# Kernel optimization log

Measured on AMD Instinct MI355X. Metric: run time of the kernel, lower is better.

## Reference

```python
import jax, jax.numpy as jnp
import numpy as np

NUM_HEADS = 16
HIDDEN = 1024
ATTN_DIM = 64            # per-head q/k dim
HEAD_OUT = 64            # per-head v dim
OUT_DIM = 1024
BATCH, SEQ = 2, 2048


def setup_inputs() -> dict:
    key = jax.random.key(0)
    ks = jax.random.split(key, 9)
    s_in = 1.0 / np.sqrt(HIDDEN)
    s_o = 1.0 / np.sqrt(NUM_HEADS * HEAD_OUT)
    return {
        "x": jax.random.normal(ks[0], (BATCH, SEQ, HIDDEN), dtype=jnp.float32),
        # Linear weights stored [in, out] so y = x @ W + b
        "Wq": jax.random.uniform(ks[1], (HIDDEN, NUM_HEADS * ATTN_DIM), jnp.float32, -s_in, s_in),
        "bq": jax.random.uniform(ks[2], (NUM_HEADS * ATTN_DIM,), jnp.float32, -s_in, s_in),
        "Wk": jax.random.uniform(ks[3], (HIDDEN, NUM_HEADS * ATTN_DIM), jnp.float32, -s_in, s_in),
        "bk": jax.random.uniform(ks[4], (NUM_HEADS * ATTN_DIM,), jnp.float32, -s_in, s_in),
        "Wv": jax.random.uniform(ks[5], (HIDDEN, NUM_HEADS * HEAD_OUT), jnp.float32, -s_in, s_in),
        "bv": jax.random.uniform(ks[6], (HIDDEN, NUM_HEADS * HEAD_OUT)[1:], jnp.float32, -s_in, s_in),
        "Wo": jax.random.uniform(ks[7], (NUM_HEADS * HEAD_OUT, OUT_DIM), jnp.float32, -s_o, s_o),
        "bo": jax.random.uniform(ks[8], (OUT_DIM,), jnp.float32, -s_o, s_o),
    }


def _split_heads(y, h):
    b, s, _ = y.shape
    return y.reshape(b, s, h, -1).transpose(0, 2, 1, 3)  # [b, h, s, d]


def reference(x, Wq, bq, Wk, bk, Wv, bv, Wo, bo):
    h = NUM_HEADS
    q = _split_heads(x @ Wq + bq, h)                    # [b,h,s,dq]
    k = _split_heads(x @ Wk + bk, h)                    # [b,h,s,dq]
    v = _split_heads(x @ Wv + bv, h)                    # [b,h,s,dv]
    scale = 1.0 / jnp.sqrt(jnp.float32(ATTN_DIM))
    # pattern[b,h,i,j] = key_i . query_j  (i=key index, j=query index)
    pattern = jnp.einsum('bhid,bhjd->bhij', k, q) * scale
    # softmax over key axis (dim=-2), matching t.softmax(..., dim=-2)
    prob = jax.nn.softmax(pattern, axis=-2)             # [b,h,key,query]
    # out[b,h,s,d] = sum_i prob[b,h,i,s] * v[b,h,i,d]
    out = jnp.einsum('bhis,bhid->bhsd', prob, v)        # [b,h,s,dv]
    b, _, s, dv = out.shape
    concat = out.transpose(0, 2, 1, 3).reshape(b, s, h * dv)
    return concat @ Wo + bo
```

## Files before the change

kernel.cpp:

```cpp
#include <hip/hip_runtime.h>
#include <cstdint>
#include <cstddef>

using f16   = _Float16;
using f16x4 = __attribute__((ext_vector_type(4))) _Float16;
using f16x8 = __attribute__((ext_vector_type(8))) _Float16;
using f32x4 = __attribute__((ext_vector_type(4))) float;

__device__ __forceinline__ f32x4 mfma16(f16x8 a, f16x8 b, f32x4 c) {
  return __builtin_amdgcn_mfma_f32_16x16x32_f16(a, b, c, 0, 0, 0);
}

__device__ __forceinline__ void gld16(const f16* g, f16* l) {
  __builtin_amdgcn_global_load_lds(
      (__attribute__((address_space(1))) void*)g,
      (__attribute__((address_space(3))) void*)l, 16, 0, 0);
}

constexpr int BATCH = 2, SEQL = 2048, HID = 1024, NH = 16, DH = 64;
constexpr int TOK = BATCH * SEQL;
constexpr int NQKV = 3 * HID;

__global__ __launch_bounds__(256) void k_convert_x(const float* __restrict__ x,
                                                   f16* __restrict__ xh) {
  int i = (blockIdx.x * 256 + threadIdx.x) * 4;
  float4 v = *(const float4*)(x + i);
  f16x4 o = { (f16)v.x, (f16)v.y, (f16)v.z, (f16)v.w };
  *(f16x4*)(xh + i) = o;
}

__global__ __launch_bounds__(256) void k_transpose(const float* __restrict__ Wq,
                                                   const float* __restrict__ Wk,
                                                   const float* __restrict__ Wv,
                                                   const float* __restrict__ Wo,
                                                   f16* __restrict__ WT,
                                                   f16* __restrict__ WoT) {
  __shared__ float tile[32][33];
  int mat = blockIdx.z;
  const float* W = (mat == 0) ? Wq : (mat == 1) ? Wk : (mat == 2) ? Wv : Wo;
  int in0 = blockIdx.x * 32, out0 = blockIdx.y * 32;
  int c = threadIdx.x & 31, r8 = threadIdx.x >> 5;
#pragma unroll
  for (int i = 0; i < 4; i++) {
    int r = r8 + i * 8;
    tile[r][c] = W[(size_t)(in0 + r) * HID + out0 + c];
  }
  __syncthreads();
#pragma unroll
  for (int i = 0; i < 4; i++) {
    int r = r8 + i * 8;
    f16 v = (f16)tile[c][r];
    if (mat == 3) WoT[(size_t)(out0 + r) * HID + in0 + c] = v;
    else          WT[(size_t)(mat * HID + out0 + r) * HID + in0 + c] = v;
  }
}

__global__ __launch_bounds__(256, 2) void k_gemm_qkv(
    const f16* __restrict__ xh, const f16* __restrict__ WT,
    const float* __restrict__ bq, const float* __restrict__ bk,
    const float* __restrict__ bv,
    f16* __restrict__ Qh, f16* __restrict__ Kh, f16* __restrict__ Vp) {
  constexpr int K = HID;
  int m0 = blockIdx.x * 128, n0 = blockIdx.y * 128;
  int tid = threadIdx.x;
  int w = tid >> 6, lane = tid & 63, lr = lane & 15, lq = lane >> 4;
  int wm = w >> 1, wn = w & 1;
  __shared__ f16 Ash[128 * 32];
  __shared__ f16 Bsh[128 * 32];
  f32x4 acc[4][4];
#pragma unroll
  for (int i = 0; i < 4; i++)
#pragma unroll
    for (int j = 0; j < 4; j++) acc[i][j] = (f32x4){0.f, 0.f, 0.f, 0.f};

  int row0 = tid >> 2, seg0 = tid & 3;
  int row1 = (256 + tid) >> 2;
  const f16* Ag0 = xh + (size_t)(m0 + row0) * K + seg0 * 8;
  const f16* Ag1 = xh + (size_t)(m0 + row1) * K + seg0 * 8;
  const f16* Bg0 = WT + (size_t)(n0 + row0) * K + seg0 * 8;
  const f16* Bg1 = WT + (size_t)(n0 + row1) * K + seg0 * 8;

  for (int k0 = 0; k0 < K; k0 += 32) {
    __syncthreads();
    gld16(Ag0 + k0, Ash + tid * 8);
    gld16(Ag1 + k0, Ash + (256 + tid) * 8);
    gld16(Bg0 + k0, Bsh + tid * 8);
    gld16(Bg1 + k0, Bsh + (256 + tid) * 8);
    __syncthreads();
    f16x8 af[4], bfr[4];
#pragma unroll
    for (int mt = 0; mt < 4; mt++)
      af[mt] = *(const f16x8*)(Ash + (wm * 64 + mt * 16 + lr) * 32 + lq * 8);
#pragma unroll
    for (int nt = 0; nt < 4; nt++)
      bfr[nt] = *(const f16x8*)(Bsh + (wn * 64 + nt * 16 + lr) * 32 + lq * 8);
#pragma unroll
    for (int mt = 0; mt < 4; mt++)
#pragma unroll
      for (int nt = 0; nt < 4; nt++)
        acc[mt][nt] = mfma16(af[mt], bfr[nt], acc[mt][nt]);
  }

#pragma unroll
  for (int nt = 0; nt < 4; nt++) {
    int o = n0 + wn * 64 + nt * 16 + lr;
    int sec = o >> 10, o1 = o & 1023, hh = o1 >> 6, dd = o1 & 63;
    float bias = (sec == 0) ? bq[o1] : (sec == 1) ? bk[o1] : bv[o1];
#pragma unroll
    for (int mt = 0; mt < 4; mt++) {
      int t0 = m0 + wm * 64 + mt * 16 + lq * 4;
      int b = t0 >> 11, s0 = t0 & (SEQL - 1);
      size_t bh = (size_t)(b * NH + hh);
      if (sec == 2) {
        f16x4 pv = { (f16)(acc[mt][nt][0] + bias), (f16)(acc[mt][nt][1] + bias),
                     (f16)(acc[mt][nt][2] + bias), (f16)(acc[mt][nt][3] + bias) };
        int pb = (s0 & ~31) | ((s0 & 12) << 1) | ((s0 >> 2) & 4);
        *(f16x4*)(Vp + (bh * DH + dd) * SEQL + pb) = pv;
      } else {
        f16* dst = (sec == 0) ? Qh : Kh;
#pragma unroll
        for (int r = 0; r < 4; r++)
          dst[(bh * SEQL + s0 + r) * DH + dd] = (f16)(acc[mt][nt][r] + bias);
      }
    }
  }
}

__global__ __launch_bounds__(256, 2) void k_attn(const f16* __restrict__ Qh,
                                                 const f16* __restrict__ Kh,
                                                 const f16* __restrict__ Vp,
                                                 f16* __restrict__ Ao) {
  int bh = blockIdx.x;
  int qblk = blockIdx.y;
  int b = bh >> 4, h = bh & 15;
  int tid = threadIdx.x;
  int w = tid >> 6;
  int g = w >> 1;
  int wq = w & 1;
  int lane = tid & 63, lr = lane & 15, lq = lane >> 4;

  __shared__ f16 sh[8 * 64 * 64];

  f16x8 qf[4][2];
#pragma unroll
  for (int qt = 0; qt < 4; qt++) {
    const f16* Qbase =
        Qh + ((size_t)bh * SEQL + qblk * 128 + wq * 64 + qt * 16 + lr) * DH;
#pragma unroll
    for (int ks = 0; ks < 2; ks++) {
      qf[qt][ks] = *(const f16x8*)(Qbase + ks * 32 + lq * 8);
      qf[qt][ks] = qf[qt][ks] * (f16)0.18033688f;
    }
  }

  f32x4 O[4][4];
#pragma unroll
  for (int qt = 0; qt < 4; qt++)
#pragma unroll
    for (int dt = 0; dt < 4; dt++) O[qt][dt] = (f32x4){0.f, 0.f, 0.f, 0.f};
  float lsum[4] = {0.f, 0.f, 0.f, 0.f};

  int sg = w >> 1, skv = w & 1;
  int srow8 = lane >> 3;
  int scol = ((lane & 7) ^ srow8) * 8;
  const f16* sgl;
  size_t pstride, kbstride;
  if (skv == 0) {
    sgl = Kh + ((size_t)bh * SEQL + sg * 1024 + srow8) * DH + scol;
    pstride = (size_t)8 * DH;
    kbstride = (size_t)64 * DH;
  } else {
    sgl = Vp + ((size_t)bh * DH + srow8) * SEQL + sg * 1024 + scol;
    pstride = (size_t)8 * SEQL;
    kbstride = (size_t)64;
  }
  f16* sdst0 = sh + ((sg * 2 + 0) * 2 + skv) * 4096 + lane * 8;
  f16* sdst1 = sh + ((sg * 2 + 1) * 2 + skv) * 4096 + lane * 8;

  int swz = lr & 7;
  int c0 = ((0 * 4 + lq) ^ swz) * 8;
  int c1 = ((1 * 4 + lq) ^ swz) * 8;

  {
    const f16* src = sgl;
#pragma unroll
    for (int p8 = 0; p8 < 8; p8++) gld16(src + p8 * pstride, sdst0 + p8 * 512);
  }

  for (int kb = 0; kb < 16; kb++) {
    __syncthreads();
    if (kb < 15) {
      const f16* src = sgl + (size_t)(kb + 1) * kbstride;
      f16* sdst = ((kb + 1) & 1) ? sdst1 : sdst0;
#pragma unroll
      for (int p8 = 0; p8 < 8; p8++) gld16(src + p8 * pstride, sdst + p8 * 512);
    }

    const f16* Kp = sh + ((g * 2 + (kb & 1)) * 2 + 0) * 4096;
    const f16* Vq = Kp + 4096;

    f32x4 sacc[4][4];
#pragma unroll
    for (int qt = 0; qt < 4; qt++)
#pragma unroll
      for (int kt = 0; kt < 4; kt++) sacc[qt][kt] = (f32x4){0.f, 0.f, 0.f, 0.f};
    __builtin_amdgcn_s_setprio(1);
#pragma unroll
    for (int ks = 0; ks < 2; ks++) {
      int kc = ks ? c1 : c0;
#pragma unroll
      for (int kt = 0; kt < 4; kt++) {
        f16x8 kf = *(const f16x8*)(Kp + (kt * 16 + lr) * 64 + kc);
        sacc[0][kt] = mfma16(kf, qf[0][ks], sacc[0][kt]);
        sacc[1][kt] = mfma16(kf, qf[1][ks], sacc[1][kt]);
        sacc[2][kt] = mfma16(kf, qf[2][ks], sacc[2][kt]);
        sacc[3][kt] = mfma16(kf, qf[3][ks], sacc[3][kt]);
      }
    }
    __builtin_amdgcn_s_setprio(0);

    f16x8 pf[4][2];
#pragma unroll
    for (int qt = 0; qt < 4; qt++) {
      float part = 0.f;
#pragma unroll
      for (int kt = 0; kt < 4; kt++) {
        float p0 = __builtin_amdgcn_exp2f(sacc[qt][kt][0]);
        float p1 = __builtin_amdgcn_exp2f(sacc[qt][kt][1]);
        float p2 = __builtin_amdgcn_exp2f(sacc[qt][kt][2]);
        float p3 = __builtin_amdgcn_exp2f(sacc[qt][kt][3]);
        part += (p0 + p1) + (p2 + p3);
        int s = kt >> 1, off = (kt & 1) * 4;
        pf[qt][s][off + 0] = (f16)p0; pf[qt][s][off + 1] = (f16)p1;
        pf[qt][s][off + 2] = (f16)p2; pf[qt][s][off + 3] = (f16)p3;
      }
      lsum[qt] += part;
    }

    __builtin_amdgcn_s_setprio(1);
#pragma unroll
    for (int s = 0; s < 2; s++) {
      int vc = s ? c1 : c0;
#pragma unroll
      for (int dt = 0; dt < 4; dt++) {
        f16x8 vf = *(const f16x8*)(Vq + (dt * 16 + lr) * 64 + vc);
        O[0][dt] = mfma16(vf, pf[0][s], O[0][dt]);
        O[1][dt] = mfma16(vf, pf[1][s], O[1][dt]);
        O[2][dt] = mfma16(vf, pf[2][s], O[2][dt]);
        O[3][dt] = mfma16(vf, pf[3][s], O[3][dt]);
      }
    }
    __builtin_amdgcn_s_setprio(0);
  }

  __syncthreads();
  float* part = (float*)sh;
  float* plsum = part + 128 * 64;
  if (g == 1) {
#pragma unroll
    for (int qt = 0; qt < 4; qt++) {
      int ql = wq * 64 + qt * 16 + lr;
#pragma unroll
      for (int dt = 0; dt < 4; dt++) {
        int slot = (dt * 4 + lq) ^ lr;
        *(f32x4*)(part + ql * 64 + slot * 4) = O[qt][dt];
      }
      plsum[ql * 4 + lq] = lsum[qt];
    }
  }
  __syncthreads();
  if (g == 0) {
#pragma unroll
    for (int qt = 0; qt < 4; qt++) {
      int ql = wq * 64 + qt * 16 + lr;
      float ls = lsum[qt] + plsum[ql * 4 + lq];
      float l1 = ls + __shfl_xor(ls, 16);
      float ltot = l1 + __shfl_xor(l1, 32);
      float inv = 1.0f / ltot;
      int q = qblk * 128 + ql;
      f16* dst = Ao + ((size_t)b * SEQL + q) * HID + h * DH;
#pragma unroll
      for (int dt = 0; dt < 4; dt++) {
        int slot = (dt * 4 + lq) ^ lr;
        f32x4 po = *(const f32x4*)(part + ql * 64 + slot * 4);
        f16x4 o = { (f16)((O[qt][dt][0] + po[0]) * inv),
                    (f16)((O[qt][dt][1] + po[1]) * inv),
                    (f16)((O[qt][dt][2] + po[2]) * inv),
                    (f16)((O[qt][dt][3] + po[3]) * inv) };
        *(f16x4*)(dst + dt * 16 + lq * 4) = o;
      }
    }
  }
}

__global__ __launch_bounds__(256, 2) void k_gemm_out(const f16* __restrict__ Ah,
                                                     const f16* __restrict__ WoT,
                                                     const float* __restrict__ bo,
                                                     float* __restrict__ out) {
  constexpr int K = HID;
  int m0 = blockIdx.x * 128, n0 = blockIdx.y * 64;
  int tid = threadIdx.x;
  int w = tid >> 6, lane = tid & 63, lr = lane & 15, lq = lane >> 4;
  int wm = w >> 1, wn = w & 1;
  __shared__ f16 Ash[128 * 32];
  __shared__ f16 Bsh[64 * 32];
  f32x4 acc[4][2];
#pragma unroll
  for (int i = 0; i < 4; i++)
#pragma unroll
    for (int j = 0; j < 2; j++) acc[i][j] = (f32x4){0.f, 0.f, 0.f, 0.f};

  int row0 = tid >> 2, seg0 = tid & 3;
  int row1 = (256 + tid) >> 2;
  const f16* Ag0 = Ah + (size_t)(m0 + row0) * K + seg0 * 8;
  const f16* Ag1 = Ah + (size_t)(m0 + row1) * K + seg0 * 8;
  const f16* Bg0 = WoT + (size_t)(n0 + row0) * K + seg0 * 8;

  for (int k0 = 0; k0 < K; k0 += 32) {
    __syncthreads();
    gld16(Ag0 + k0, Ash + tid * 8);
    gld16(Ag1 + k0, Ash + (256 + tid) * 8);
    gld16(Bg0 + k0, Bsh + tid * 8);
    __syncthreads();
    f16x8 af[4], bfr[2];
#pragma unroll
    for (int mt = 0; mt < 4; mt++)
      af[mt] = *(const f16x8*)(Ash + (wm * 64 + mt * 16 + lr) * 32 + lq * 8);
#pragma unroll
    for (int nt = 0; nt < 2; nt++)
      bfr[nt] = *(const f16x8*)(Bsh + (wn * 32 + nt * 16 + lr) * 32 + lq * 8);
#pragma unroll
    for (int mt = 0; mt < 4; mt++)
#pragma unroll
      for (int nt = 0; nt < 2; nt++)
        acc[mt][nt] = mfma16(af[mt], bfr[nt], acc[mt][nt]);
  }

#pragma unroll
  for (int nt = 0; nt < 2; nt++) {
    int o = n0 + wn * 32 + nt * 16 + lr;
    float bias = bo[o];
#pragma unroll
    for (int mt = 0; mt < 4; mt++) {
      int t0 = m0 + wm * 64 + mt * 16 + lq * 4;
#pragma unroll
      for (int r = 0; r < 4; r++)
        out[(size_t)(t0 + r) * HID + o] = acc[mt][nt][r] + bias;
    }
  }
}

extern "C" void kernel_launch(void* const* d_in, const int* in_sizes, int n_in,
                              void* d_out, int out_size, void* d_ws, size_t ws_size,
                              hipStream_t stream) {
  const float* x  = (const float*)d_in[0];
  const float* Wq = (const float*)d_in[1];
  const float* bq = (const float*)d_in[2];
  const float* Wk = (const float*)d_in[3];
  const float* bk = (const float*)d_in[4];
  const float* Wv = (const float*)d_in[5];
  const float* bv = (const float*)d_in[6];
  const float* Wo = (const float*)d_in[7];
  const float* bo = (const float*)d_in[8];

  char* ws = (char*)d_ws;
  f16* xh  = (f16*)(ws + 0);
  f16* WT  = (f16*)(ws + 8388608);
  f16* WoT = (f16*)(ws + 14680064);
  f16* Qh  = (f16*)(ws + 16777216);
  f16* Kh  = (f16*)(ws + 25165824);
  f16* Vp  = (f16*)(ws + 33554432);
  f16* Ao  = (f16*)(ws + 41943040);

  k_convert_x<<<TOK * HID / 1024, 256, 0, stream>>>(x, xh);
  k_transpose<<<dim3(32, 32, 4), 256, 0, stream>>>(Wq, Wk, Wv, Wo, WT, WoT);
  k_gemm_qkv<<<dim3(TOK / 128, NQKV / 128), 256, 0, stream>>>(xh, WT, bq, bk, bv,
                                                              Qh, Kh, Vp);
  k_attn<<<dim3(BATCH * NH, SEQL / 128), 256, 0, stream>>>(Qh, Kh, Vp, Ao);
  k_gemm_out<<<dim3(TOK / 128, HID / 64), 256, 0, stream>>>(Ao, WoT, bo,
                                                            (float*)d_out);
}
```

Before: 180.8 us.

## Fuse all stages into one persistent kernel with software grid barriers

Replaces the five separate launches (convert, transpose, QKV GEMM, attention, output GEMM) with one persistent kernel of 512 blocks that loops over each stage's work items and separates stages with an atomic-counter grid barrier. This aims to remove kernel launch gaps and tail drain between stages. It relies on all 512 blocks being co-resident, and adds barrier spin cost plus a memset for the barrier state.

```diff
diff --git a/kernel.cpp b/kernel.cpp
--- a/kernel.cpp
+++ b/kernel.cpp
@@ -20,332 +20,356 @@
 constexpr int BATCH = 2, SEQL = 2048, HID = 1024, NH = 16, DH = 64;
 constexpr int TOK = BATCH * SEQL;
 constexpr int NQKV = 3 * HID;
-
-__global__ __launch_bounds__(256) void k_convert_x(const float* __restrict__ x,
-                                                   f16* __restrict__ xh) {
-  int i = (blockIdx.x * 256 + threadIdx.x) * 4;
-  float4 v = *(const float4*)(x + i);
-  f16x4 o = { (f16)v.x, (f16)v.y, (f16)v.z, (f16)v.w };
-  *(f16x4*)(xh + i) = o;
-}
-
-__global__ __launch_bounds__(256) void k_transpose(const float* __restrict__ Wq,
-                                                   const float* __restrict__ Wk,
-                                                   const float* __restrict__ Wv,
-                                                   const float* __restrict__ Wo,
-                                                   f16* __restrict__ WT,
-                                                   f16* __restrict__ WoT) {
-  __shared__ float tile[32][33];
-  int mat = blockIdx.z;
-  const float* W = (mat == 0) ? Wq : (mat == 1) ? Wk : (mat == 2) ? Wv : Wo;
-  int in0 = blockIdx.x * 32, out0 = blockIdx.y * 32;
-  int c = threadIdx.x & 31, r8 = threadIdx.x >> 5;
-#pragma unroll
-  for (int i = 0; i < 4; i++) {
-    int r = r8 + i * 8;
-    tile[r][c] = W[(size_t)(in0 + r) * HID + out0 + c];
+constexpr int NBLK = 512;
+
+__device__ __forceinline__ void gbar(unsigned* bar) {
+  __syncthreads();
+  if (threadIdx.x == 0) {
+    __threadfence();
+    unsigned gen = __hip_atomic_load(bar + 1, __ATOMIC_ACQUIRE,
+                                     __HIP_MEMORY_SCOPE_AGENT);
+    unsigned arr = __hip_atomic_fetch_add(bar, 1u, __ATOMIC_ACQ_REL,
+                                          __HIP_MEMORY_SCOPE_AGENT);
+    if (arr == NBLK - 1) {
+      __hip_atomic_store(bar, 0u, __ATOMIC_RELAXED, __HIP_MEMORY_SCOPE_AGENT);
+      __hip_atomic_fetch_add(bar + 1, 1u, __ATOMIC_RELEASE,
+                             __HIP_MEMORY_SCOPE_AGENT);
+    } else {
+      while (__hip_atomic_load(bar + 1, __ATOMIC_ACQUIRE,
+                               __HIP_MEMORY_SCOPE_AGENT) == gen)
+        __builtin_amdgcn_s_sleep(8);
+    }
+    __threadfence();
   }
   __syncthreads();
-#pragma unroll
-  for (int i = 0; i < 4; i++) {
-    int r = r8 + i * 8;
-    f16 v = (f16)tile[c][r];
-    if (mat == 3) WoT[(size_t)(out0 + r) * HID + in0 + c] = v;
-    else          WT[(size_t)(mat * HID + out0 + r) * HID + in0 + c] = v;
+}
+
+__global__ __launch_bounds__(256, 2) void k_fused(
+    const float* __restrict__ x,  const float* __restrict__ Wq,
+    const float* __restrict__ bq, const float* __restrict__ Wk,
+    const float* __restrict__ bk, const float* __restrict__ Wv,
+    const float* __restrict__ bv, const float* __restrict__ Wo,
+    const float* __restrict__ bo, float* __restrict__ out,
+    f16* __restrict__ xh, f16* __restrict__ WT, f16* __restrict__ WoT,
+    f16* __restrict__ Qh, f16* __restrict__ Kh, f16* __restrict__ Vp,
+    f16* __restrict__ Ao, unsigned* __restrict__ bar) {
+  __shared__ __attribute__((aligned(16))) char smem[65536];
+  int bid = blockIdx.x;
+  int tid = threadIdx.x;
+
+  {
+    float (*tile)[33] = (float(*)[33])smem;
+    for (int j = bid; j < 8192; j += NBLK) {
+      if (j < 4096) {
+        int i = j * 1024 + tid * 4;
+        float4 v = *(const float4*)(x + i);
+        f16x4 o = { (f16)v.x, (f16)v.y, (f16)v.z, (f16)v.w };
+        *(f16x4*)(xh + i) = o;
+      } else {
+        int t = j - 4096;
+        int mat = t >> 10, rem = t & 1023;
+        int in0 = (rem >> 5) * 32, out0 = (rem & 31) * 32;
+        const float* W = (mat == 0) ? Wq : (mat == 1) ? Wk
+                        : (mat == 2) ? Wv : Wo;
+        int c = tid & 31, r8 = tid >> 5;
+        __syncthreads();
+#pragma unroll
+        for (int i = 0; i < 4; i++) {
+          int r = r8 + i * 8;
+          tile[r][c] = W[(size_t)(in0 + r) * HID + out0 + c];
+        }
+        __syncthreads();
+#pragma unroll
+        for (int i = 0; i < 4; i++) {
+          int r = r8 + i * 8;
+          f16 v = (f16)tile[c][r];
+          if (mat == 3) WoT[(size_t)(out0 + r) * HID + in0 + c] = v;
+          else          WT[(size_t)(mat * HID + out0 + r) * HID + in0 + c] = v;
+        }
+      }
+    }
   }
-}
-
-__global__ __launch_bounds__(256, 2) void k_gemm_qkv(
-    const f16* __restrict__ xh, const f16* __restrict__ WT,
-    const float* __restrict__ bq, const float* __restrict__ bk,
-    const float* __restrict__ bv,
-    f16* __restrict__ Qh, f16* __restrict__ Kh, f16* __restrict__ Vp) {
-  constexpr int K = HID;
-  int m0 = blockIdx.x * 128, n0 = blockIdx.y * 128;
-  int tid = threadIdx.x;
-  int w = tid >> 6, lane = tid & 63, lr = lane & 15, lq = lane >> 4;
-  int wm = w >> 1, wn = w & 1;
-  __shared__ f16 Ash[128 * 32];
-  __shared__ f16 Bsh[128 * 32];
-  f32x4 acc[4][4];
-#pragma unroll
-  for (int i = 0; i < 4; i++)
-#pragma unroll
-    for (int j = 0; j < 4; j++) acc[i][j] = (f32x4){0.f, 0.f, 0.f, 0.f};
-
-  int row0 = tid >> 2, seg0 = tid & 3;
-  int row1 = (256 + tid) >> 2;
-  const f16* Ag0 = xh + (size_t)(m0 + row0) * K + seg0 * 8;
-  const f16* Ag1 = xh + (size_t)(m0 + row1) * K + seg0 * 8;
-  const f16* Bg0 = WT + (size_t)(n0 + row0) * K + seg0 * 8;
-  const f16* Bg1 = WT + (size_t)(n0 + row1) * K + seg0 * 8;
-
-  for (int k0 = 0; k0 < K; k0 += 32) {
+  gbar(bar);
+
+  {
+    f16* Ash = (f16*)smem;
+    f16* Bsh = Ash + 128 * 32;
+    int w = tid >> 6, lane = tid & 63, lr = lane & 15, lq = lane >> 4;
+    int wm = w >> 1, wn = w & 1;
+    int row0 = tid >> 2, seg0 = tid & 3;
+    int row1 = (256 + tid) >> 2;
+    for (int t = bid; t < 768; t += NBLK) {
+      int m0 = (t & 31) * 128, n0 = (t >> 5) * 128;
+      f32x4 acc[4][4];
+#pragma unroll
+      for (int i = 0; i < 4; i++)
+#pragma unroll
+        for (int j = 0; j < 4; j++) acc[i][j] = (f32x4){0.f, 0.f, 0.f, 0.f};
+
+      const f16* Ag0 = xh + (size_t)(m0 + row0) * HID + seg0 * 8;
+      const f16* Ag1 = xh + (size_t)(m0 + row1) * HID + seg0 * 8;
+      const f16* Bg0 = WT + (size_t)(n0 + row0) * HID + seg0 * 8;
+      const f16* Bg1 = WT + (size_t)(n0 + row1) * HID + seg0 * 8;
+
+      for (int k0 = 0; k0 < HID; k0 += 32) {
+        __syncthreads();
+        gld16(Ag0 + k0, Ash + tid * 8);
+        gld16(Ag1 + k0, Ash + (256 + tid) * 8);
+        gld16(Bg0 + k0, Bsh + tid * 8);
+        gld16(Bg1 + k0, Bsh + (256 + tid) * 8);
+        __syncthreads();
+        f16x8 af[4], bfr[4];
+#pragma unroll
+        for (int mt = 0; mt < 4; mt++)
+          af[mt] = *(const f16x8*)(Ash + (wm * 64 + mt * 16 + lr) * 32 + lq * 8);
+#pragma unroll
+        for (int nt = 0; nt < 4; nt++)
+          bfr[nt] = *(const f16x8*)(Bsh + (wn * 64 + nt * 16 + lr) * 32 + lq * 8);
+#pragma unroll
+        for (int mt = 0; mt < 4; mt++)
+#pragma unroll
+          for (int nt = 0; nt < 4; nt++)
+            acc[mt][nt] = mfma16(af[mt], bfr[nt], acc[mt][nt]);
+      }
+
+#pragma unroll
+      for (int nt = 0; nt < 4; nt++) {
+        int o = n0 + wn * 64 + nt * 16 + lr;
+        int sec = o >> 10, o1 = o & 1023, hh = o1 >> 6, dd = o1 & 63;
+        float bias = (sec == 0) ? bq[o1] : (sec == 1) ? bk[o1] : bv[o1];
+#pragma unroll
+        for (int mt = 0; mt < 4; mt++) {
+          int t0 = m0 + wm * 64 + mt * 16 + lq * 4;
+          int b = t0 >> 11, s0 = t0 & (SEQL - 1);
+          size_t bh = (size_t)(b * NH + hh);
+          if (sec == 2) {
+            f16x4 pv = { (f16)(acc[mt][nt][0] + bias),
+                         (f16)(acc[mt][nt][1] + bias),
+                         (f16)(acc[mt][nt][2] + bias),
+                         (f16)(acc[mt][nt][3] + bias) };
+            int pb = (s0 & ~31) | ((s0 & 12) << 1) | ((s0 >> 2) & 4);
+            *(f16x4*)(Vp + (bh * DH + dd) * SEQL + pb) = pv;
+          } else {
+            f16* dst = (sec == 0) ? Qh : Kh;
+#pragma unroll
+            for (int r = 0; r < 4; r++)
+              dst[(bh * SEQL + s0 + r) * DH + dd] = (f16)(acc[mt][nt][r] + bias);
+          }
+        }
+      }
+    }
+  }
+  gbar(bar);
+
+  {
+    int bh = bid & 31;
+    int qblk = bid >> 5;
+    int b = bh >> 4, h = bh & 15;
+    int w = tid >> 6;
+    int g = w >> 1;
+    int wq = w & 1;
+    int lane = tid & 63, lr = lane & 15, lq = lane >> 4;
+    f16* sh = (f16*)smem;
+
+    f16x8 qf[4][2];
+#pragma unroll
+    for (int qt = 0; qt < 4; qt++) {
+      const f16* Qbase =
+          Qh + ((size_t)bh * SEQL + qblk * 128 + wq * 64 + qt * 16 + lr) * DH;
+#pragma unroll
+      for (int ks = 0; ks < 2; ks++) {
+        qf[qt][ks] = *(const f16x8*)(Qbase + ks * 32 + lq * 8);
+        qf[qt][ks] = qf[qt][ks] * (f16)0.18033688f;
+      }
+    }
+
+    f32x4 O[4][4];
+#pragma unroll
+    for (int qt = 0; qt < 4; qt++)
+#pragma unroll
+      for (int dt = 0; dt < 4; dt++) O[qt][dt] = (f32x4){0.f, 0.f, 0.f, 0.f};
+    float lsum[4] = {0.f, 0.f, 0.f, 0.f};
+
+    int sg = w >> 1, kv = w & 1;
+    int srow8 = lane >> 3;
+    int scol = ((lane & 7) ^ srow8) * 8;
+    const f16* sgl;
+    size_t pstride, kbstride;
+    if (kv == 0) {
+      sgl = Kh + ((size_t)bh * SEQL + sg * 1024 + srow8) * DH + scol;
+      pstride = (size_t)8 * DH;
+      kbstride = (size_t)64 * DH;
+    } else {
+      sgl = Vp + ((size_t)bh * DH + srow8) * SEQL + sg * 1024 + scol;
+      pstride = (size_t)8 * SEQL;
+      kbstride = (size_t)64;
+    }
+    f16* sdst0 = sh + ((sg * 2 + 0) * 2 + kv) * 4096 + lane * 8;
+    f16* sdst1 = sh + ((sg * 2 + 1) * 2 + kv) * 4096 + lane * 8;
+
+    int swz = lr & 7;
+    int c0 = ((0 * 4 + lq) ^ swz) * 8;
+    int c1 = ((1 * 4 + lq) ^ swz) * 8;
+
+#pragma unroll
+    for (int p8 = 0; p8 < 8; p8++) gld16(sgl + p8 * pstride, sdst0 + p8 * 512);
+
+    for (int kb = 0; kb < 16; kb++) {
+      __syncthreads();
+      if (kb < 15) {
+        const f16* src = sgl + (size_t)(kb + 1) * kbstride;
+        f16* sd = ((kb + 1) & 1) ? sdst1 : sdst0;
+#pragma unroll
+        for (int p8 = 0; p8 < 8; p8++) gld16(src + p8 * pstride, sd + p8 * 512);
+      }
+
+      const f16* Kp = sh + ((g * 2 + (kb & 1)) * 2 + 0) * 4096;
+      const f16* Vq = Kp + 4096;
+
+      f32x4 sacc[4][4];
+#pragma unroll
+      for (int qt = 0; qt < 4; qt++)
+#pragma unroll
+        for (int kt = 0; kt < 4; kt++) sacc[qt][kt] = (f32x4){0.f, 0.f, 0.f, 0.f};
+      __builtin_amdgcn_s_setprio(1);
+#pragma unroll
+      for (int ks = 0; ks < 2; ks++) {
+        int kc = ks ? c1 : c0;
+#pragma unroll
+        for (int kt = 0; kt < 4; kt++) {
+          f16x8 kf = *(const f16x8*)(Kp + (kt * 16 + lr) * 64 + kc);
+          sacc[0][kt] = mfma16(kf, qf[0][ks], sacc[0][kt]);
+          sacc[1][kt] = mfma16(kf, qf[1][ks], sacc[1][kt]);
+          sacc[2][kt] = mfma16(kf, qf[2][ks], sacc[2][kt]);
+          sacc[3][kt] = mfma16(kf, qf[3][ks], sacc[3][kt]);
+        }
+      }
+      __builtin_amdgcn_s_setprio(0);
+
+      f16x8 pf[4][2];
+#pragma unroll
+      for (int qt = 0; qt < 4; qt++) {
+        float part = 0.f;
+#pragma unroll
+        for (int kt = 0; kt < 4; kt++) {
+          float p0 = __builtin_amdgcn_exp2f(sacc[qt][kt][0]);
+          float p1 = __builtin_amdgcn_exp2f(sacc[qt][kt][1]);
+          float p2 = __builtin_amdgcn_exp2f(sacc[qt][kt][2]);
+          float p3 = __builtin_amdgcn_exp2f(sacc[qt][kt][3]);
+          part += (p0 + p1) + (p2 + p3);
+          int s = kt >> 1, off = (kt & 1) * 4;
+          pf[qt][s][off + 0] = (f16)p0; pf[qt][s][off + 1] = (f16)p1;
+          pf[qt][s][off + 2] = (f16)p2; pf[qt][s][off + 3] = (f16)p3;
+        }
+        lsum[qt] += part;
+      }
+
+      __builtin_amdgcn_s_setprio(1);
+#pragma unroll
+      for (int s = 0; s < 2; s++) {
+        int vc = s ? c1 : c0;
+#pragma unroll
+        for (int dt = 0; dt < 4; dt++) {
+          f16x8 vf = *(const f16x8*)(Vq + (dt * 16 + lr) * 64 + vc);
+          O[0][dt] = mfma16(vf, pf[0][s], O[0][dt]);
+          O[1][dt] = mfma16(vf, pf[1][s], O[1][dt]);
+          O[2][dt] = mfma16(vf, pf[2][s], O[2][dt]);
+          O[3][dt] = mfma16(vf, pf[3][s], O[3][dt]);
+        }
+      }
+      __builtin_amdgcn_s_setprio(0);
+    }
+
     __syncthreads();
-    gld16(Ag0 + k0, Ash + tid * 8);
-    gld16(Ag1 + k0, Ash + (256 + tid) * 8);
-    gld16(Bg0 + k0, Bsh + tid * 8);
-    gld16(Bg1 + k0, Bsh + (256 + tid) * 8);
+    float* mrg = (float*)sh;
+    float* pls = mrg + 128 * 64;
+    if (g == 1) {
+#pragma unroll
+      for (int qt = 0; qt < 4; qt++) {
+        int ql = wq * 64 + qt * 16 + lr;
+#pragma unroll
+        for (int dt = 0; dt < 4; dt++) {
+          int slot = (dt * 4 + lq) ^ lr;
+          *(f32x4*)(mrg + ql * 64 + slot * 4) = O[qt][dt];
+        }
+        pls[ql * 4 + lq] = lsum[qt];
+      }
+    }
     __syncthreads();
-    f16x8 af[4], bfr[4];
-#pragma unroll
-    for (int mt = 0; mt < 4; mt++)
-      af[mt] = *(const f16x8*)(Ash + (wm * 64 + mt * 16 + lr) * 32 + lq * 8);
-#pragma unroll
-    for (int nt = 0; nt < 4; nt++)
-      bfr[nt] = *(const f16x8*)(Bsh + (wn * 64 + nt * 16 + lr) * 32 + lq * 8);
-#pragma unroll
-    for (int mt = 0; mt < 4; mt++)
-#pragma unroll
-      for (int nt = 0; nt < 4; nt++)
-        acc[mt][nt] = mfma16(af[mt], bfr[nt], acc[mt][nt]);
+    if (g == 0) {
+#pragma unroll
+      for (int qt = 0; qt < 4; qt++) {
+        int ql = wq * 64 + qt * 16 + lr;
+        float ls = lsum[qt] + pls[ql * 4 + lq];
+        float l1 = ls + __shfl_xor(ls, 16);
+        float ltot = l1 + __shfl_xor(l1, 32);
+        float inv = 1.0f / ltot;
+        int q = qblk * 128 + ql;
+        f16* dst = Ao + ((size_t)b * SEQL + q) * HID + h * DH;
+#pragma unroll
+        for (int dt = 0; dt < 4; dt++) {
+          int slot = (dt * 4 + lq) ^ lr;
+          f32x4 po = *(const f32x4*)(mrg + ql * 64 + slot * 4);
+          f16x4 o = { (f16)((O[qt][dt][0] + po[0]) * inv),
+                      (f16)((O[qt][dt][1] + po[1]) * inv),
+                      (f16)((O[qt][dt][2] + po[2]) * inv),
+                      (f16)((O[qt][dt][3] + po[3]) * inv) };
+          *(f16x4*)(dst + dt * 16 + lq * 4) = o;
+        }
+      }
+    }
   }
-
-#pragma unroll
-  for (int nt = 0; nt < 4; nt++) {
-    int o = n0 + wn * 64 + nt * 16 + lr;
-    int sec = o >> 10, o1 = o & 1023, hh = o1 >> 6, dd = o1 & 63;
-    float bias = (sec == 0) ? bq[o1] : (sec == 1) ? bk[o1] : bv[o1];
-#pragma unroll
-    for (int mt = 0; mt < 4; mt++) {
-      int t0 = m0 + wm * 64 + mt * 16 + lq * 4;
-      int b = t0 >> 11, s0 = t0 & (SEQL - 1);
-      size_t bh = (size_t)(b * NH + hh);
-      if (sec == 2) {
-        f16x4 pv = { (f16)(acc[mt][nt][0] + bias), (f16)(acc[mt][nt][1] + bias),
-                     (f16)(acc[mt][nt][2] + bias), (f16)(acc[mt][nt][3] + bias) };
-        int pb = (s0 & ~31) | ((s0 & 12) << 1) | ((s0 >> 2) & 4);
-        *(f16x4*)(Vp + (bh * DH + dd) * SEQL + pb) = pv;
-      } else {
-        f16* dst = (sec == 0) ? Qh : Kh;
+  gbar(bar);
+
+  {
+    f16* Ash = (f16*)smem;
+    f16* Bsh = Ash + 128 * 32;
+    int w = tid >> 6, lane = tid & 63, lr = lane & 15, lq = lane >> 4;
+    int wm = w >> 1, wn = w & 1;
+    int m0 = (bid & 31) * 128, n0 = (bid >> 5) * 64;
+    f32x4 acc[4][2];
+#pragma unroll
+    for (int i = 0; i < 4; i++)
+#pragma unroll
+      for (int j = 0; j < 2; j++) acc[i][j] = (f32x4){0.f, 0.f, 0.f, 0.f};
+
+    int row0 = tid >> 2, seg0 = tid & 3;
+    int row1 = (256 + tid) >> 2;
+    const f16* Ag0 = Ao + (size_t)(m0 + row0) * HID + seg0 * 8;
+    const f16* Ag1 = Ao + (size_t)(m0 + row1) * HID + seg0 * 8;
+    const f16* Bg0 = WoT + (size_t)(n0 + row0) * HID + seg0 * 8;
+
+    for (int k0 = 0; k0 < HID; k0 += 32) {
+      __syncthreads();
+      gld16(Ag0 + k0, Ash + tid * 8);
+      gld16(Ag1 + k0, Ash + (256 + tid) * 8);
+      gld16(Bg0 + k0, Bsh + tid * 8);
+      __syncthreads();
+      f16x8 af[4], bfr[2];
+#pragma unroll
+      for (int mt = 0; mt < 4; mt++)
+        af[mt] = *(const f16x8*)(Ash + (wm * 64 + mt * 16 + lr) * 32 + lq * 8);
+#pragma unroll
+      for (int nt = 0; nt < 2; nt++)
+        bfr[nt] = *(const f16x8*)(Bsh + (wn * 32 + nt * 16 + lr) * 32 + lq * 8);
+#pragma unroll
+      for (int mt = 0; mt < 4; mt++)
+#pragma unroll
+        for (int nt = 0; nt < 2; nt++)
+          acc[mt][nt] = mfma16(af[mt], bfr[nt], acc[mt][nt]);
+    }
+
+#pragma unroll
+    for (int nt = 0; nt < 2; nt++) {
+      int o = n0 + wn * 32 + nt * 16 + lr;
+      float bias = bo[o];
+#pragma unroll
+      for (int mt = 0; mt < 4; mt++) {
+        int t0 = m0 + wm * 64 + mt * 16 + lq * 4;
 #pragma unroll
         for (int r = 0; r < 4; r++)
-          dst[(bh * SEQL + s0 + r) * DH + dd] = (f16)(acc[mt][nt][r] + bias);
-      }
-    }
-  }
-}
-
-__global__ __launch_bounds__(256, 2) void k_attn(const f16* __restrict__ Qh,
-                                                 const f16* __restrict__ Kh,
-                                                 const f16* __restrict__ Vp,
-                                                 f16* __restrict__ Ao) {
-  int bh = blockIdx.x;
-  int qblk = blockIdx.y;
-  int b = bh >> 4, h = bh & 15;
-  int tid = threadIdx.x;
-  int w = tid >> 6;
-  int g = w >> 1;
-  int wq = w & 1;
-  int lane = tid & 63, lr = lane & 15, lq = lane >> 4;
-
-  __shared__ f16 sh[8 * 64 * 64];
-
-  f16x8 qf[4][2];
-#pragma unroll
-  for (int qt = 0; qt < 4; qt++) {
-    const f16* Qbase =
-        Qh + ((size_t)bh * SEQL + qblk * 128 + wq * 64 + qt * 16 + lr) * DH;
-#pragma unroll
-    for (int ks = 0; ks < 2; ks++) {
-      qf[qt][ks] = *(const f16x8*)(Qbase + ks * 32 + lq * 8);
-      qf[qt][ks] = qf[qt][ks] * (f16)0.18033688f;
-    }
-  }
-
-  f32x4 O[4][4];
-#pragma unroll
-  for (int qt = 0; qt < 4; qt++)
-#pragma unroll
-    for (int dt = 0; dt < 4; dt++) O[qt][dt] = (f32x4){0.f, 0.f, 0.f, 0.f};
-  float lsum[4] = {0.f, 0.f, 0.f, 0.f};
-
-  int sg = w >> 1, skv = w & 1;
-  int srow8 = lane >> 3;
-  int scol = ((lane & 7) ^ srow8) * 8;
-  const f16* sgl;
-  size_t pstride, kbstride;
-  if (skv == 0) {
-    sgl = Kh + ((size_t)bh * SEQL + sg * 1024 + srow8) * DH + scol;
-    pstride = (size_t)8 * DH;
-    kbstride = (size_t)64 * DH;
-  } else {
-    sgl = Vp + ((size_t)bh * DH + srow8) * SEQL + sg * 1024 + scol;
-    pstride = (size_t)8 * SEQL;
-    kbstride = (size_t)64;
-  }
-  f16* sdst0 = sh + ((sg * 2 + 0) * 2 + skv) * 4096 + lane * 8;
-  f16* sdst1 = sh + ((sg * 2 + 1) * 2 + skv) * 4096 + lane * 8;
-
-  int swz = lr & 7;
-  int c0 = ((0 * 4 + lq) ^ swz) * 8;
-  int c1 = ((1 * 4 + lq) ^ swz) * 8;
-
-  {
-    const f16* src = sgl;
-#pragma unroll
-    for (int p8 = 0; p8 < 8; p8++) gld16(src + p8 * pstride, sdst0 + p8 * 512);
-  }
-
-  for (int kb = 0; kb < 16; kb++) {
-    __syncthreads();
-    if (kb < 15) {
-      const f16* src = sgl + (size_t)(kb + 1) * kbstride;
-      f16* sdst = ((kb + 1) & 1) ? sdst1 : sdst0;
-#pragma unroll
-      for (int p8 = 0; p8 < 8; p8++) gld16(src + p8 * pstride, sdst + p8 * 512);
-    }
-
-    const f16* Kp = sh + ((g * 2 + (kb & 1)) * 2 + 0) * 4096;
-    const f16* Vq = Kp + 4096;
-
-    f32x4 sacc[4][4];
-#pragma unroll
-    for (int qt = 0; qt < 4; qt++)
-#pragma unroll
-      for (int kt = 0; kt < 4; kt++) sacc[qt][kt] = (f32x4){0.f, 0.f, 0.f, 0.f};
-    __builtin_amdgcn_s_setprio(1);
-#pragma unroll
-    for (int ks = 0; ks < 2; ks++) {
-      int kc = ks ? c1 : c0;
-#pragma unroll
-      for (int kt = 0; kt < 4; kt++) {
-        f16x8 kf = *(const f16x8*)(Kp + (kt * 16 + lr) * 64 + kc);
-        sacc[0][kt] = mfma16(kf, qf[0][ks], sacc[0][kt]);
-        sacc[1][kt] = mfma16(kf, qf[1][ks], sacc[1][kt]);
-        sacc[2][kt] = mfma16(kf, qf[2][ks], sacc[2][kt]);
-        sacc[3][kt] = mfma16(kf, qf[3][ks], sacc[3][kt]);
-      }
-    }
-    __builtin_amdgcn_s_setprio(0);
-
-    f16x8 pf[4][2];
-#pragma unroll
-    for (int qt = 0; qt < 4; qt++) {
-      float part = 0.f;
-#pragma unroll
-      for (int kt = 0; kt < 4; kt++) {
-        float p0 = __builtin_amdgcn_exp2f(sacc[qt][kt][0]);
-        float p1 = __builtin_amdgcn_exp2f(sacc[qt][kt][1]);
-        float p2 = __builtin_amdgcn_exp2f(sacc[qt][kt][2]);
-        float p3 = __builtin_amdgcn_exp2f(sacc[qt][kt][3]);
-        part += (p0 + p1) + (p2 + p3);
-        int s = kt >> 1, off = (kt & 1) * 4;
-        pf[qt][s][off + 0] = (f16)p0; pf[qt][s][off + 1] = (f16)p1;
-        pf[qt][s][off + 2] = (f16)p2; pf[qt][s][off + 3] = (f16)p3;
-      }
-      lsum[qt] += part;
-    }
-
-    __builtin_amdgcn_s_setprio(1);
-#pragma unroll
-    for (int s = 0; s < 2; s++) {
-      int vc = s ? c1 : c0;
-#pragma unroll
-      for (int dt = 0; dt < 4; dt++) {
-        f16x8 vf = *(const f16x8*)(Vq + (dt * 16 + lr) * 64 + vc);
-        O[0][dt] = mfma16(vf, pf[0][s], O[0][dt]);
-        O[1][dt] = mfma16(vf, pf[1][s], O[1][dt]);
-        O[2][dt] = mfma16(vf, pf[2][s], O[2][dt]);
-        O[3][dt] = mfma16(vf, pf[3][s], O[3][dt]);
-      }
-    }
-    __builtin_amdgcn_s_setprio(0);
-  }
-
-  __syncthreads();
-  float* part = (float*)sh;
-  float* plsum = part + 128 * 64;
-  if (g == 1) {
-#pragma unroll
-    for (int qt = 0; qt < 4; qt++) {
-      int ql = wq * 64 + qt * 16 + lr;
-#pragma unroll
-      for (int dt = 0; dt < 4; dt++) {
-        int slot = (dt * 4 + lq) ^ lr;
-        *(f32x4*)(part + ql * 64 + slot * 4) = O[qt][dt];
-      }
-      plsum[ql * 4 + lq] = lsum[qt];
-    }
-  }
-  __syncthreads();
-  if (g == 0) {
-#pragma unroll
-    for (int qt = 0; qt < 4; qt++) {
-      int ql = wq * 64 + qt * 16 + lr;
-      float ls = lsum[qt] + plsum[ql * 4 + lq];
-      float l1 = ls + __shfl_xor(ls, 16);
-      float ltot = l1 + __shfl_xor(l1, 32);
-      float inv = 1.0f / ltot;
-      int q = qblk * 128 + ql;
-      f16* dst = Ao + ((size_t)b * SEQL + q) * HID + h * DH;
-#pragma unroll
-      for (int dt = 0; dt < 4; dt++) {
-        int slot = (dt * 4 + lq) ^ lr;
-        f32x4 po = *(const f32x4*)(part + ql * 64 + slot * 4);
-        f16x4 o = { (f16)((O[qt][dt][0] + po[0]) * inv),
-                    (f16)((O[qt][dt][1] + po[1]) * inv),
-                    (f16)((O[qt][dt][2] + po[2]) * inv),
-                    (f16)((O[qt][dt][3] + po[3]) * inv) };
-        *(f16x4*)(dst + dt * 16 + lq * 4) = o;
-      }
-    }
-  }
-}
-
-__global__ __launch_bounds__(256, 2) void k_gemm_out(const f16* __restrict__ Ah,
-                                                     const f16* __restrict__ WoT,
-                                                     const float* __restrict__ bo,
-                                                     float* __restrict__ out) {
-  constexpr int K = HID;
-  int m0 = blockIdx.x * 128, n0 = blockIdx.y * 64;
-  int tid = threadIdx.x;
-  int w = tid >> 6, lane = tid & 63, lr = lane & 15, lq = lane >> 4;
-  int wm = w >> 1, wn = w & 1;
-  __shared__ f16 Ash[128 * 32];
-  __shared__ f16 Bsh[64 * 32];
-  f32x4 acc[4][2];
-#pragma unroll
-  for (int i = 0; i < 4; i++)
-#pragma unroll
-    for (int j = 0; j < 2; j++) acc[i][j] = (f32x4){0.f, 0.f, 0.f, 0.f};
-
-  int row0 = tid >> 2, seg0 = tid & 3;
-  int row1 = (256 + tid) >> 2;
-  const f16* Ag0 = Ah + (size_t)(m0 + row0) * K + seg0 * 8;
-  const f16* Ag1 = Ah + (size_t)(m0 + row1) * K + seg0 * 8;
-  const f16* Bg0 = WoT + (size_t)(n0 + row0) * K + seg0 * 8;
-
-  for (int k0 = 0; k0 < K; k0 += 32) {
-    __syncthreads();
-    gld16(Ag0 + k0, Ash + tid * 8);
-    gld16(Ag1 + k0, Ash + (256 + tid) * 8);
-    gld16(Bg0 + k0, Bsh + tid * 8);
-    __syncthreads();
-    f16x8 af[4], bfr[2];
-#pragma unroll
-    for (int mt = 0; mt < 4; mt++)
-      af[mt] = *(const f16x8*)(Ash + (wm * 64 + mt * 16 + lr) * 32 + lq * 8);
-#pragma unroll
-    for (int nt = 0; nt < 2; nt++)
-      bfr[nt] = *(const f16x8*)(Bsh + (wn * 32 + nt * 16 + lr) * 32 + lq * 8);
-#pragma unroll
-    for (int mt = 0; mt < 4; mt++)
-#pragma unroll
-      for (int nt = 0; nt < 2; nt++)
-        acc[mt][nt] = mfma16(af[mt], bfr[nt], acc[mt][nt]);
-  }
-
-#pragma unroll
-  for (int nt = 0; nt < 2; nt++) {
-    int o = n0 + wn * 32 + nt * 16 + lr;
-    float bias = bo[o];
-#pragma unroll
-    for (int mt = 0; mt < 4; mt++) {
-      int t0 = m0 + wm * 64 + mt * 16 + lq * 4;
-#pragma unroll
-      for (int r = 0; r < 4; r++)
-        out[(size_t)(t0 + r) * HID + o] = acc[mt][nt][r] + bias;
+          out[(size_t)(t0 + r) * HID + o] = acc[mt][nt][r] + bias;
+      }
     }
   }
 }
@@ -371,12 +395,10 @@
   f16* Kh  = (f16*)(ws + 25165824);
   f16* Vp  = (f16*)(ws + 33554432);
   f16* Ao  = (f16*)(ws + 41943040);
-
-  k_convert_x<<<TOK * HID / 1024, 256, 0, stream>>>(x, xh);
-  k_transpose<<<dim3(32, 32, 4), 256, 0, stream>>>(Wq, Wk, Wv, Wo, WT, WoT);
-  k_gemm_qkv<<<dim3(TOK / 128, NQKV / 128), 256, 0, stream>>>(xh, WT, bq, bk, bv,
-                                                              Qh, Kh, Vp);
-  k_attn<<<dim3(BATCH * NH, SEQL / 128), 256, 0, stream>>>(Qh, Kh, Vp, Ao);
-  k_gemm_out<<<dim3(TOK / 128, HID / 64), 256, 0, stream>>>(Ao, WoT, bo,
-                                                            (float*)d_out);
+  unsigned* bar = (unsigned*)(ws + 50331648);
+
+  hipMemsetAsync(bar, 0, 64, stream);
+  k_fused<<<NBLK, 256, 0, stream>>>(x, Wq, bq, Wk, bk, Wv, bv, Wo, bo,
+                                    (float*)d_out, xh, WT, WoT, Qh, Kh, Vp,
+                                    Ao, bar);
 }
```

New measurement: 503.0 us. +178.2%, slower.
